# Performance work log

Hardware: AMD Instinct MI355X
Metric: run time of the kernel (lower is better)

## Reference

```python
import jax, jax.numpy as jnp
import numpy as np

HEAD_DIM = 64
N_Q_HEADS = 32
N_KV_HEADS = 8
EXPAND = N_Q_HEADS // N_KV_HEADS  # 4
ROPE_THETA = 10000.0
COMP_RATIO = 0.5
VOCAB = 32000
D_MODEL = 2048


def rotate_half(x):
    x1, x2 = jnp.split(x, 2, axis=-1)
    return jnp.concatenate([-x2, x1], axis=-1)


def setup_inputs() -> dict:
    key = jax.random.key(0)
    k0, k1, k2, k3 = jax.random.split(key, 4)
    input_ids = jax.random.randint(k0, (1, 2048), 0, VOCAB, dtype=jnp.int64)
    embed_table = jax.random.normal(k1, (VOCAB, D_MODEL), dtype=jnp.float32) * 0.02
    Wq = jax.random.normal(k2, (N_Q_HEADS * HEAD_DIM, D_MODEL), dtype=jnp.float32) * 0.02
    Wk = jax.random.normal(k3, (N_KV_HEADS * HEAD_DIM, D_MODEL), dtype=jnp.float32) * 0.02
    return {"input_ids": input_ids, "embed_table": embed_table, "Wq": Wq, "Wk": Wk}


def reference(input_ids, embed_table, Wq, Wk):
    B, S = input_ids.shape
    x = embed_table[input_ids]  # [B,S,D]

    # projections (torch Linear: x @ W.T), split heads -> [B,H,S,hd]
    q = jnp.einsum('bsd,ed->bse', x, Wq).reshape(B, S, N_Q_HEADS, HEAD_DIM).transpose(0, 2, 1, 3)
    k = jnp.einsum('bsd,ed->bse', x, Wk).reshape(B, S, N_KV_HEADS, HEAD_DIM).transpose(0, 2, 1, 3)

    # Llama RoPE, position_ids = arange(S)
    pos = jnp.arange(S, dtype=jnp.float32)
    inv_freq = 1.0 / (ROPE_THETA ** (jnp.arange(0, HEAD_DIM, 2, dtype=jnp.float32) / HEAD_DIM))
    freqs = pos[:, None] * inv_freq[None, :]                 # [S, hd/2]
    emb = jnp.concatenate([freqs, freqs], axis=-1)           # [S, hd]
    cos = jnp.cos(emb)[None, None]                           # [1,1,S,hd]
    sin = jnp.sin(emb)[None, None]
    q = q * cos + rotate_half(q) * sin
    k = k * cos + rotate_half(k) * sin

    # GQA expansion (repeat_interleave over head dim)
    k = jnp.repeat(k, EXPAND, axis=1)                        # [B,Hq,S,hd]

    # NOTE: original applies NO 1/sqrt(head_dim) scaling and NO causal mask to scores
    scores = jnp.einsum('bhqd,bhkd->bhqk', q, k)             # [B,H,S,S]
    attn = jax.nn.softmax(scores, axis=-1)

    importance = attn.mean(axis=1).mean(axis=1)[0]           # [S]

    klen = max(int(S * COMP_RATIO), 2)
    _, topk_ids = jax.lax.top_k(importance, klen)
    topk_ids = jnp.sort(topk_ids)
    # static-shape version of the "append last token if missing" branch:
    # always append S-1 (duplicate if already selected)
    topk_full = jnp.concatenate([topk_ids, jnp.array([S - 1], dtype=topk_ids.dtype)])
    pruned = jnp.take_along_axis(input_ids, topk_full[None, :], axis=1)
    return pruned, topk_full
```

## Files before the change

### kernel.cpp

```cpp
#include <hip/hip_runtime.h>
#include <math.h>

#define S       2048
#define D       2048
#define EQ      2048
#define EK      512
#define ETOT    2560
#define NH      32
#define NKV     8
#define HD      64
#define KLEN    1024

#define OFF_COS   ((size_t)0)
#define OFF_SIN   ((size_t)(256u << 10))
#define OFF_QK    ((size_t)(1u << 20))
#define OFF_KF1   ((size_t)(22u << 20))
#define OFF_KF2   ((size_t)(24u << 20))
#define OFF_PART  ((size_t)(26u << 20))
#define OFF_VALS  ((size_t)(34u << 20))
#define OFF_FLAGS ((size_t)((34u << 20) + (16u << 10)))
#define OFF_ACCP  ((size_t)((34u << 20) + (32u << 10)))

__global__ void trig_kernel(float* __restrict__ cosT, float* __restrict__ sinT) {
  int idx = blockIdx.x * blockDim.x + threadIdx.x;
  int s = idx >> 5, i = idx & 31;
  double invf = 1.0 / pow(10000.0, (double)i / 32.0);
  double ang = (double)s * invf;
  cosT[idx] = (float)cos(ang);
  sinT[idx] = (float)sin(ang);
}

#define PBM 128
#define PBN 128
#define PBK 32
#define NKT (D / PBK)

typedef _Float16 f16x8 __attribute__((ext_vector_type(8)));
typedef float    f32x4 __attribute__((ext_vector_type(4)));

__global__ __launch_bounds__(256, 2) void proj_gemm_mfma(
    const int* __restrict__ ids, const float* __restrict__ embed,
    const float* __restrict__ Wq, const float* __restrict__ Wk,
    float* __restrict__ C) {
  __shared__ __attribute__((aligned(16))) _Float16 sA[2][2][PBM * PBK];
  __shared__ __attribute__((aligned(16))) _Float16 sB[2][2][PBN * PBK];
  const int t = threadIdx.x;
  const int col0 = blockIdx.x * PBN;
  const int row0 = blockIdx.y * PBM;
  const float* Wbase = (col0 < EQ) ? (Wq + (size_t)col0 * D)
                                   : (Wk + (size_t)(col0 - EQ) * D);

  const float* srcA[2];
  const float* srcB[2];
  int ldsOff[2];
#pragma unroll
  for (int q = 0; q < 2; ++q) {
    const int e = t + q * 256;
    const int lane = e & 63, rt = e >> 6;
    const int r = rt * 16 + (lane & 15);
    const int koff = (lane >> 4) * 8;
    srcA[q] = embed + (size_t)ids[row0 + r] * D + koff;
    srcB[q] = Wbase + (size_t)r * D + koff;
    ldsOff[q] = e * 8;
  }

  const int ln = t & 63, w = t >> 6;
  const int wm = w >> 1, wn = w & 1;
  const int aoff = ln * 8;

  f32x4 acc[4][4];
#pragma unroll
  for (int m = 0; m < 4; ++m)
#pragma unroll
    for (int n = 0; n < 4; ++n) {
      f32x4 z = {0.f, 0.f, 0.f, 0.f};
      acc[m][n] = z;
    }

  float4 va[2][2], vb[2][2];

  auto load_regs = [&](int k) {
#pragma unroll
    for (int q = 0; q < 2; ++q) {
      va[q][0] = *(const float4*)(srcA[q] + k);
      va[q][1] = *(const float4*)(srcA[q] + k + 4);
      vb[q][0] = *(const float4*)(srcB[q] + k);
      vb[q][1] = *(const float4*)(srcB[q] + k + 4);
    }
  };

  auto cvt_write = [&](int buf) {
#pragma unroll
    for (int q = 0; q < 2; ++q) {
      const float fa[8] = {va[q][0].x, va[q][0].y, va[q][0].z, va[q][0].w,
                           va[q][1].x, va[q][1].y, va[q][1].z, va[q][1].w};
      const float fb[8] = {vb[q][0].x, vb[q][0].y, vb[q][0].z, vb[q][0].w,
                           vb[q][1].x, vb[q][1].y, vb[q][1].z, vb[q][1].w};
      f16x8 ah1, ah2, bh1, bh2;
#pragma unroll
      for (int j = 0; j < 8; ++j) {
        float fs = fa[j] * 64.f;
        _Float16 h = (_Float16)fs;
        ah1[j] = h;
        ah2[j] = (_Float16)(fs - (float)h);
        fs = fb[j] * 64.f;
        h = (_Float16)fs;
        bh1[j] = h;
        bh2[j] = (_Float16)(fs - (float)h);
      }
      *(f16x8*)&sA[buf][0][ldsOff[q]] = ah1;
      *(f16x8*)&sA[buf][1][ldsOff[q]] = ah2;
      *(f16x8*)&sB[buf][0][ldsOff[q]] = bh1;
      *(f16x8*)&sB[buf][1][ldsOff[q]] = bh2;
    }
  };

  load_regs(0);
  cvt_write(0);
  __syncthreads();

  int cur = 0;
  for (int kt = 0; kt < NKT; ++kt) {
    const int nb = cur ^ 1;
    const bool more = (kt + 1 < NKT);
    if (more) load_regs((kt + 1) * PBK);

    f16x8 a1[4], a2[4], b1[4], b2[4];
#pragma unroll
    for (int m = 0; m < 4; ++m) {
      const int c = (wm * 4 + m) * (16 * PBK) + aoff;
      a1[m] = *(const f16x8*)&sA[cur][0][c];
      a2[m] = *(const f16x8*)&sA[cur][1][c];
    }
#pragma unroll
    for (int n = 0; n < 4; ++n) {
      const int c = (wn * 4 + n) * (16 * PBK) + aoff;
      b1[n] = *(const f16x8*)&sB[cur][0][c];
      b2[n] = *(const f16x8*)&sB[cur][1][c];
    }
#pragma unroll
    for (int m = 0; m < 4; ++m)
#pragma unroll
      for (int n = 0; n < 4; ++n) {
        acc[m][n] = __builtin_amdgcn_mfma_f32_16x16x32_f16(a1[m], b1[n], acc[m][n], 0, 0, 0);
        acc[m][n] = __builtin_amdgcn_mfma_f32_16x16x32_f16(a1[m], b2[n], acc[m][n], 0, 0, 0);
        acc[m][n] = __builtin_amdgcn_mfma_f32_16x16x32_f16(a2[m], b1[n], acc[m][n], 0, 0, 0);
      }

    if (more) cvt_write(nb);
    __syncthreads();
    cur = nb;
  }

  const float inv = 1.f / 4096.f;
  const int colb = col0 + wn * 64 + (ln & 15);
  const int rowb = row0 + wm * 64 + (ln >> 4) * 4;
#pragma unroll
  for (int m = 0; m < 4; ++m)
#pragma unroll
    for (int j = 0; j < 4; ++j) {
      float* dst = C + (size_t)(rowb + m * 16 + j) * ETOT + colb;
#pragma unroll
      for (int n = 0; n < 4; ++n) dst[n * 16] = acc[m][n][j] * inv;
    }
}

__global__ void rope_q_kernel(float* __restrict__ qk,
                              const float* __restrict__ cosT,
                              const float* __restrict__ sinT) {
  int idx = blockIdx.x * blockDim.x + threadIdx.x;
  int s = idx >> 10;
  int rem = idx & 1023;
  int h = rem >> 5, i = rem & 31;
  float c = cosT[(s << 5) + i], sn = sinT[(s << 5) + i];
  float* p = qk + (size_t)s * ETOT + h * HD + i;
  float x1 = p[0], x2 = p[32];
  p[0]  = fmaf(x1, c, -x2 * sn);
  p[32] = fmaf(x2, c,  x1 * sn);
}

__global__ __launch_bounds__(256) void rope_k_kernel(
    const float* __restrict__ qk, _Float16* __restrict__ kf1,
    _Float16* __restrict__ kf2,
    const float* __restrict__ cosT, const float* __restrict__ sinT) {
  __shared__ float tile[64][65];
  __shared__ __attribute__((aligned(16))) float rot[64][68];
  __shared__ float ct[64][33];
  __shared__ float st[64][33];
  const int kv = blockIdx.x;
  const int s0 = blockIdx.y * 64;
  const int t = threadIdx.x;
  {
    const int c = t & 63, r = t >> 6;
#pragma unroll
    for (int p = 0; p < 16; ++p)
      tile[r + 4 * p][c] = qk[(size_t)(s0 + r + 4 * p) * ETOT + EQ + kv * HD + c];
  }
  {
    const int i = t & 31, r = t >> 5;
#pragma unroll
    for (int p = 0; p < 8; ++p) {
      ct[r + 8 * p][i] = cosT[(s0 + r + 8 * p) * 32 + i];
      st[r + 8 * p][i] = sinT[(s0 + r + 8 * p) * 32 + i];
    }
  }
  __syncthreads();
  {
    const int s = t & 63, dbase = t >> 6;
#pragma unroll
    for (int p = 0; p < 16; ++p) {
      const int d = dbase + 4 * p;
      float v;
      if (d < 32) {
        const float c = ct[s][d], sn = st[s][d];
        const float x1 = tile[s][d], x2 = tile[s][d + 32];
        v = fmaf(x1, c, -x2 * sn);
      } else {
        const float c = ct[s][d - 32], sn = st[s][d - 32];
        const float x1 = tile[s][d - 32], x2 = tile[s][d];
        v = fmaf(x2, c, x1 * sn);
      }
      rot[s][d] = v;
    }
  }
  __syncthreads();
  {
    const int w = t >> 6, l = t & 63;
    const int jt_g = (s0 >> 4) + w;
    const int jl = w * 16 + (l & 15);
#pragma unroll
    for (int ks = 0; ks < 2; ++ks) {
      const int d0 = ks * 32 + (l >> 4) * 8;
      const float4 v0 = *(const float4*)&rot[jl][d0];
      const float4 v1 = *(const float4*)&rot[jl][d0 + 4];
      const float f[8] = {v0.x, v0.y, v0.z, v0.w, v1.x, v1.y, v1.z, v1.w};
      f16x8 h1, h2;
#pragma unroll
      for (int i = 0; i < 8; ++i) {
        float fs = f[i] * 64.f;
        _Float16 hh = (_Float16)fs;
        h1[i] = hh;
        h2[i] = (_Float16)(fs - (float)hh);
      }
      const size_t off = (((size_t)(kv * 128 + jt_g) * 2 + ks) * 64 + l) * 8;
      *(f16x8*)&kf1[off] = h1;
      *(f16x8*)&kf2[off] = h2;
    }
  }
}

__global__ __launch_bounds__(512) void attn_mfma2(
    const float* __restrict__ qk, const _Float16* __restrict__ kf1,
    const _Float16* __restrict__ kf2, float* __restrict__ part) {
  const int h = blockIdx.x;
  const int rb = blockIdx.y;
  const int kv = h >> 2;
  const int t = threadIdx.x;
  const int l = t & 63, w = t >> 6;
  const int lo8 = l * 8;
  __shared__ __attribute__((aligned(16))) _Float16 kbuf[4 * 2 * 2 * 64 * 8];
  __shared__ float sbuf[8][64];

  f16x8 a1[2], a2[2];
  {
    const int grow = rb * 128 + w * 16 + (l & 15);
    const float* src = qk + (size_t)grow * ETOT + h * HD + ((l >> 4) * 8);
#pragma unroll
    for (int ks = 0; ks < 2; ++ks) {
      const float4 v0 = *(const float4*)(src + ks * 32);
      const float4 v1 = *(const float4*)(src + ks * 32 + 4);
      const float f[8] = {v0.x, v0.y, v0.z, v0.w, v1.x, v1.y, v1.z, v1.w};
#pragma unroll
      for (int i = 0; i < 8; ++i) {
        float fs = f[i] * 64.f;
        _Float16 hh = (_Float16)fs;
        a1[ks][i] = hh;
        a2[ks][i] = (_Float16)(fs - (float)hh);
      }
    }
  }

  const _Float16* gp[2];
  int ldsoff[2];
#pragma unroll
  for (int i = 0; i < 2; ++i) {
    const int c = 2 * w + i;
    const int tl = c >> 2, sp = (c >> 1) & 1, ks = c & 1;
    gp[i] = (sp ? kf2 : kf1) +
            ((size_t)((kv * 128 + tl) * 2 + ks)) * 512 + lo8;
    ldsoff[i] = ((tl * 2 + sp) * 2 + ks) * 512 + lo8;
  }

  uint4 stg0, stg1;
  auto LD = [&](int step) {
    stg0 = *(const uint4*)(gp[0] + (size_t)step * 4096);
    stg1 = *(const uint4*)(gp[1] + (size_t)step * 4096);
  };
  auto WR = [&]() {
    *(uint4*)&kbuf[ldsoff[0]] = stg0;
    *(uint4*)&kbuf[ldsoff[1]] = stg1;
  };

  float rsacc[4] = {0.f, 0.f, 0.f, 0.f};
  float invZ[4] = {0.f, 0.f, 0.f, 0.f};
  const int prow = h * 16 + rb;

  LD(0); WR();
  for (int ph = 0; ph < 2; ++ph) {
    for (int it = 0; it < 32; ++it) {
      const int nxt = (it + 1) & 31;
      const bool more = !(ph == 1 && it == 31);
      if (more) LD(nxt);
      __syncthreads();
      float v0t = 0.f, v1t = 0.f, v2t = 0.f, v3t = 0.f;
#pragma unroll
      for (int tl = 0; tl < 4; ++tl) {
        const f16x8 b1k0 = *(const f16x8*)&kbuf[((tl * 2 + 0) * 2 + 0) * 512 + lo8];
        const f16x8 b1k1 = *(const f16x8*)&kbuf[((tl * 2 + 0) * 2 + 1) * 512 + lo8];
        const f16x8 b2k0 = *(const f16x8*)&kbuf[((tl * 2 + 1) * 2 + 0) * 512 + lo8];
        const f16x8 b2k1 = *(const f16x8*)&kbuf[((tl * 2 + 1) * 2 + 1) * 512 + lo8];
        f32x4 a = {0.f, 0.f, 0.f, 0.f};
        a = __builtin_amdgcn_mfma_f32_16x16x32_f16(a1[0], b1k0, a, 0, 0, 0);
        a = __builtin_amdgcn_mfma_f32_16x16x32_f16(a1[0], b2k0, a, 0, 0, 0);
        a = __builtin_amdgcn_mfma_f32_16x16x32_f16(a2[0], b1k0, a, 0, 0, 0);
        a = __builtin_amdgcn_mfma_f32_16x16x32_f16(a1[1], b1k1, a, 0, 0, 0);
        a = __builtin_amdgcn_mfma_f32_16x16x32_f16(a1[1], b2k1, a, 0, 0, 0);
        a = __builtin_amdgcn_mfma_f32_16x16x32_f16(a2[1], b1k1, a, 0, 0, 0);
        if (ph == 0) {
#pragma unroll
          for (int r = 0; r < 4; ++r) {
            const float s = a[r] * (1.f / 4096.f);
            const float e = fmaf(s, fmaf(s, fmaf(s, fmaf(s, 1.f / 24.f, 1.f / 6.f),
                                                 0.5f), 1.f), 1.f);
            rsacc[r] += e;
          }
        } else {
          float vv = 0.f;
#pragma unroll
          for (int r = 0; r < 4; ++r) {
            const float s = a[r] * (1.f / 4096.f);
            const float e = fmaf(s, fmaf(s, fmaf(s, fmaf(s, 1.f / 24.f, 1.f / 6.f),
                                                 0.5f), 1.f), 1.f);
            vv = fmaf(e, invZ[r], vv);
          }
          if (tl == 0) v0t = vv;
          else if (tl == 1) v1t = vv;
          else if (tl == 2) v2t = vv;
          else v3t = vv;
        }
      }
      if (ph == 1) {
        float m0 = v0t + __shfl_xor(v0t, 16, 64);
        float m1 = v1t + __shfl_xor(v1t, 16, 64);
        float m2 = v2t + __shfl_xor(v2t, 16, 64);
        float m3 = v3t + __shfl_xor(v3t, 16, 64);
        const bool b4 = (l & 16) != 0;
        float a01 = b4 ? m1 : m0;
        float a23 = b4 ? m3 : m2;
        a01 += __shfl_xor(a01, 32, 64);
        a23 += __shfl_xor(a23, 32, 64);
        const float wv = (l & 32) ? a23 : a01;
        sbuf[w][l] = wv;
      }
      __syncthreads();
      if (ph == 1 && w == 0) {
        float s2 = 0.f;
#pragma unroll
        for (int ww = 0; ww < 8; ++ww) s2 += sbuf[ww][l];
        part[(size_t)prow * S + it * 64 + l] = s2;
      }
      if (more) WR();
    }
    if (ph == 0) {
#pragma unroll
      for (int r = 0; r < 4; ++r) {
#pragma unroll
        for (int off = 1; off < 16; off <<= 1)
          rsacc[r] += __shfl_xor(rsacc[r], off, 64);
        invZ[r] = 1.f / rsacc[r];
      }
    }
  }
}

__global__ void vals1_kernel(const float* __restrict__ part,
                             double* __restrict__ accp) {
  int j = blockIdx.x * 256 + threadIdx.x;
  int g = blockIdx.y;
  const float* p = part + (size_t)g * 16 * S + j;
  double s = 0.0;
  for (int b = 0; b < 16; ++b) s += (double)p[(size_t)b * S];
  accp[(size_t)g * S + j] = s;
}
__global__ void vals2_kernel(const double* __restrict__ accp,
                             double* __restrict__ vals) {
  int j = blockIdx.x * 256 + threadIdx.x;
  double s = 0.0;
  for (int g = 0; g < 32; ++g) s += accp[(size_t)g * S + j];
  vals[j] = s;
}

__global__ __launch_bounds__(256) void flags_kernel(
    const double* __restrict__ vals, int* __restrict__ flags) {
  const int j = blockIdx.x;
  const int t = threadIdx.x;
  const double v = vals[j];
  int rank = 0;
  for (int j2 = t; j2 < S; j2 += 256) {
    const double v2 = vals[j2];
    rank += (v2 > v) || (v2 == v && j2 < j);
  }
#pragma unroll
  for (int off = 32; off > 0; off >>= 1) rank += __shfl_xor(rank, off, 64);
  __shared__ int red[4];
  if ((t & 63) == 0) red[t >> 6] = rank;
  __syncthreads();
  if (t == 0)
    flags[j] = ((red[0] + red[1] + red[2] + red[3]) < KLEN) ? 1 : 0;
}

__global__ __launch_bounds__(1024) void emit_kernel(
    const int* __restrict__ flags, const int* __restrict__ ids,
    int* __restrict__ out) {
  __shared__ int fl[S];
  __shared__ int csum[32];
  __shared__ int cpre[32];
  const int t = threadIdx.x;
  for (int j = t; j < S; j += 1024) fl[j] = flags[j];
  __syncthreads();
  if (t < 32) {
    int s = 0;
    for (int i = 0; i < 64; ++i) s += fl[t * 64 + i];
    csum[t] = s;
  }
  __syncthreads();
  if (t == 0) {
    int run = 0;
    for (int c = 0; c < 32; ++c) { cpre[c] = run; run += csum[c]; }
  }
  __syncthreads();
  for (int j = t; j < S; j += 1024) {
    if (fl[j]) {
      int pos = cpre[j >> 6];
      for (int j2 = j & ~63; j2 < j; ++j2) pos += fl[j2];
      out[pos] = ids[j];
      out[KLEN + 1 + pos] = j;
    }
  }
  if (t == 0) {
    out[KLEN] = ids[S - 1];
    out[KLEN + 1 + KLEN] = S - 1;
  }
}

extern "C" void kernel_launch(void* const* d_in, const int* in_sizes, int n_in,
                              void* d_out, int out_size, void* d_ws, size_t ws_size,
                              hipStream_t stream) {
  const int* ids = (const int*)d_in[0];
  const float* embed = (const float*)d_in[1];
  const float* Wq = (const float*)d_in[2];
  const float* Wk = (const float*)d_in[3];
  int* out = (int*)d_out;
  char* ws = (char*)d_ws;
  float* cosT = (float*)(ws + OFF_COS);
  float* sinT = (float*)(ws + OFF_SIN);
  float* qk   = (float*)(ws + OFF_QK);
  _Float16* kf1 = (_Float16*)(ws + OFF_KF1);
  _Float16* kf2 = (_Float16*)(ws + OFF_KF2);
  float* part = (float*)(ws + OFF_PART);
  double* vals = (double*)(ws + OFF_VALS);
  int* flags  = (int*)(ws + OFF_FLAGS);
  double* accp = (double*)(ws + OFF_ACCP);

  trig_kernel<<<256, 256, 0, stream>>>(cosT, sinT);
  proj_gemm_mfma<<<dim3(ETOT / PBN, S / PBM), 256, 0, stream>>>(ids, embed, Wq, Wk, qk);
  rope_q_kernel<<<(S * NH * 32) / 256, 256, 0, stream>>>(qk, cosT, sinT);
  rope_k_kernel<<<dim3(NKV, S / 64), 256, 0, stream>>>(qk, kf1, kf2, cosT, sinT);
  attn_mfma2<<<dim3(NH, S / 128), 512, 0, stream>>>(qk, kf1, kf2, part);
  vals1_kernel<<<dim3(S / 256, 32), 256, 0, stream>>>(part, accp);
  vals2_kernel<<<S / 256, 256, 0, stream>>>(accp, vals);
  flags_kernel<<<S, 256, 0, stream>>>(vals, flags);
  emit_kernel<<<1, 1024, 0, stream>>>(flags, ids, out);
}
```

Measured before the change: 611.8 us.

## Shrink projection GEMM tiles to 64x64 and add XCD-aware block swizzle

Cuts the projection GEMM tile from 128x128 to 64x64, which takes the grid from 320 blocks to 1280. Raises the occupancy hint to 5 blocks per CU and remaps the 1D block index so that blocks on the same XCD share row bands, which should improve L2 reuse of embedding rows. The goal is to fill the CUs better on a grid that was too small for the machine. The cost is less reuse per tile, so global and LDS traffic rise for each MFMA issued.

After: 618.4 us. About the same (+1.1%).

```diff
diff --git a/kernel.cpp b/kernel.cpp
--- a/kernel.cpp
+++ b/kernel.cpp
@@ -30,89 +30,85 @@
   sinT[idx] = (float)sin(ang);
 }
 
-#define PBM 128
-#define PBN 128
+#define PBM 64
+#define PBN 64
 #define PBK 32
 #define NKT (D / PBK)
 
 typedef _Float16 f16x8 __attribute__((ext_vector_type(8)));
 typedef float    f32x4 __attribute__((ext_vector_type(4)));
 
-__global__ __launch_bounds__(256, 2) void proj_gemm_mfma(
+__global__ __launch_bounds__(256, 5) void proj_gemm_mfma(
     const int* __restrict__ ids, const float* __restrict__ embed,
     const float* __restrict__ Wq, const float* __restrict__ Wk,
     float* __restrict__ C) {
   __shared__ __attribute__((aligned(16))) _Float16 sA[2][2][PBM * PBK];
   __shared__ __attribute__((aligned(16))) _Float16 sB[2][2][PBN * PBK];
   const int t = threadIdx.x;
-  const int col0 = blockIdx.x * PBN;
-  const int row0 = blockIdx.y * PBM;
+  const int bid = blockIdx.x;
+  const int xcd = bid & 7, idx = bid >> 3;
+  const int bx = idx % 40;
+  const int by = xcd * 4 + idx / 40;
+  const int col0 = bx * PBN;
+  const int row0 = by * PBM;
   const float* Wbase = (col0 < EQ) ? (Wq + (size_t)col0 * D)
                                    : (Wk + (size_t)(col0 - EQ) * D);
 
-  const float* srcA[2];
-  const float* srcB[2];
-  int ldsOff[2];
-#pragma unroll
-  for (int q = 0; q < 2; ++q) {
-    const int e = t + q * 256;
-    const int lane = e & 63, rt = e >> 6;
+  const float* srcA;
+  const float* srcB;
+  int ldsOff;
+  {
+    const int lane = t & 63, rt = t >> 6;
     const int r = rt * 16 + (lane & 15);
     const int koff = (lane >> 4) * 8;
-    srcA[q] = embed + (size_t)ids[row0 + r] * D + koff;
-    srcB[q] = Wbase + (size_t)r * D + koff;
-    ldsOff[q] = e * 8;
+    srcA = embed + (size_t)ids[row0 + r] * D + koff;
+    srcB = Wbase + (size_t)r * D + koff;
+    ldsOff = t * 8;
   }
 
   const int ln = t & 63, w = t >> 6;
   const int wm = w >> 1, wn = w & 1;
   const int aoff = ln * 8;
 
-  f32x4 acc[4][4];
-#pragma unroll
-  for (int m = 0; m < 4; ++m)
-#pragma unroll
-    for (int n = 0; n < 4; ++n) {
+  f32x4 acc[2][2];
+#pragma unroll
+  for (int m = 0; m < 2; ++m)
+#pragma unroll
+    for (int n = 0; n < 2; ++n) {
       f32x4 z = {0.f, 0.f, 0.f, 0.f};
       acc[m][n] = z;
     }
 
-  float4 va[2][2], vb[2][2];
+  float4 va[2], vb[2];
 
   auto load_regs = [&](int k) {
-#pragma unroll
-    for (int q = 0; q < 2; ++q) {
-      va[q][0] = *(const float4*)(srcA[q] + k);
-      va[q][1] = *(const float4*)(srcA[q] + k + 4);
-      vb[q][0] = *(const float4*)(srcB[q] + k);
-      vb[q][1] = *(const float4*)(srcB[q] + k + 4);
-    }
+    va[0] = *(const float4*)(srcA + k);
+    va[1] = *(const float4*)(srcA + k + 4);
+    vb[0] = *(const float4*)(srcB + k);
+    vb[1] = *(const float4*)(srcB + k + 4);
   };
 
   auto cvt_write = [&](int buf) {
-#pragma unroll
-    for (int q = 0; q < 2; ++q) {
-      const float fa[8] = {va[q][0].x, va[q][0].y, va[q][0].z, va[q][0].w,
-                           va[q][1].x, va[q][1].y, va[q][1].z, va[q][1].w};
-      const float fb[8] = {vb[q][0].x, vb[q][0].y, vb[q][0].z, vb[q][0].w,
-                           vb[q][1].x, vb[q][1].y, vb[q][1].z, vb[q][1].w};
-      f16x8 ah1, ah2, bh1, bh2;
-#pragma unroll
-      for (int j = 0; j < 8; ++j) {
-        float fs = fa[j] * 64.f;
-        _Float16 h = (_Float16)fs;
-        ah1[j] = h;
-        ah2[j] = (_Float16)(fs - (float)h);
-        fs = fb[j] * 64.f;
-        h = (_Float16)fs;
-        bh1[j] = h;
-        bh2[j] = (_Float16)(fs - (float)h);
-      }
-      *(f16x8*)&sA[buf][0][ldsOff[q]] = ah1;
-      *(f16x8*)&sA[buf][1][ldsOff[q]] = ah2;
-      *(f16x8*)&sB[buf][0][ldsOff[q]] = bh1;
-      *(f16x8*)&sB[buf][1][ldsOff[q]] = bh2;
-    }
+    const float fa[8] = {va[0].x, va[0].y, va[0].z, va[0].w,
+                         va[1].x, va[1].y, va[1].z, va[1].w};
+    const float fb[8] = {vb[0].x, vb[0].y, vb[0].z, vb[0].w,
+                         vb[1].x, vb[1].y, vb[1].z, vb[1].w};
+    f16x8 ah1, ah2, bh1, bh2;
+#pragma unroll
+    for (int j = 0; j < 8; ++j) {
+      float fs = fa[j] * 64.f;
+      _Float16 h = (_Float16)fs;
+      ah1[j] = h;
+      ah2[j] = (_Float16)(fs - (float)h);
+      fs = fb[j] * 64.f;
+      h = (_Float16)fs;
+      bh1[j] = h;
+      bh2[j] = (_Float16)(fs - (float)h);
+    }
+    *(f16x8*)&sA[buf][0][ldsOff] = ah1;
+    *(f16x8*)&sA[buf][1][ldsOff] = ah2;
+    *(f16x8*)&sB[buf][0][ldsOff] = bh1;
+    *(f16x8*)&sB[buf][1][ldsOff] = bh2;
   };
 
   load_regs(0);
@@ -125,23 +121,23 @@
     const bool more = (kt + 1 < NKT);
     if (more) load_regs((kt + 1) * PBK);
 
-    f16x8 a1[4], a2[4], b1[4], b2[4];
-#pragma unroll
-    for (int m = 0; m < 4; ++m) {
-      const int c = (wm * 4 + m) * (16 * PBK) + aoff;
+    f16x8 a1[2], a2[2], b1[2], b2[2];
+#pragma unroll
+    for (int m = 0; m < 2; ++m) {
+      const int c = (wm * 2 + m) * (16 * PBK) + aoff;
       a1[m] = *(const f16x8*)&sA[cur][0][c];
       a2[m] = *(const f16x8*)&sA[cur][1][c];
     }
 #pragma unroll
-    for (int n = 0; n < 4; ++n) {
-      const int c = (wn * 4 + n) * (16 * PBK) + aoff;
+    for (int n = 0; n < 2; ++n) {
+      const int c = (wn * 2 + n) * (16 * PBK) + aoff;
       b1[n] = *(const f16x8*)&sB[cur][0][c];
       b2[n] = *(const f16x8*)&sB[cur][1][c];
     }
 #pragma unroll
-    for (int m = 0; m < 4; ++m)
-#pragma unroll
-      for (int n = 0; n < 4; ++n) {
+    for (int m = 0; m < 2; ++m)
+#pragma unroll
+      for (int n = 0; n < 2; ++n) {
         acc[m][n] = __builtin_amdgcn_mfma_f32_16x16x32_f16(a1[m], b1[n], acc[m][n], 0, 0, 0);
         acc[m][n] = __builtin_amdgcn_mfma_f32_16x16x32_f16(a1[m], b2[n], acc[m][n], 0, 0, 0);
         acc[m][n] = __builtin_amdgcn_mfma_f32_16x16x32_f16(a2[m], b1[n], acc[m][n], 0, 0, 0);
@@ -153,15 +149,15 @@
   }
 
   const float inv = 1.f / 4096.f;
-  const int colb = col0 + wn * 64 + (ln & 15);
-  const int rowb = row0 + wm * 64 + (ln >> 4) * 4;
-#pragma unroll
-  for (int m = 0; m < 4; ++m)
+  const int colb = col0 + wn * 32 + (ln & 15);
+  const int rowb = row0 + wm * 32 + (ln >> 4) * 4;
+#pragma unroll
+  for (int m = 0; m < 2; ++m)
 #pragma unroll
     for (int j = 0; j < 4; ++j) {
       float* dst = C + (size_t)(rowb + m * 16 + j) * ETOT + colb;
 #pragma unroll
-      for (int n = 0; n < 4; ++n) dst[n * 16] = acc[m][n][j] * inv;
+      for (int n = 0; n < 2; ++n) dst[n * 16] = acc[m][n][j] * inv;
     }
 }
 
@@ -473,7 +469,7 @@
   double* accp = (double*)(ws + OFF_ACCP);
 
   trig_kernel<<<256, 256, 0, stream>>>(cosT, sinT);
-  proj_gemm_mfma<<<dim3(ETOT / PBN, S / PBM), 256, 0, stream>>>(ids, embed, Wq, Wk, qk);
+  proj_gemm_mfma<<<(S / PBM) * (ETOT / PBN), 256, 0, stream>>>(ids, embed, Wq, Wk, qk);
   rope_q_kernel<<<(S * NH * 32) / 256, 256, 0, stream>>>(qk, cosT, sinT);
   rope_k_kernel<<<dim3(NKV, S / 64), 256, 0, stream>>>(qk, kf1, kf2, cosT, sinT);
   attn_mfma2<<<dim3(NH, S / 128), 512, 0, stream>>>(qk, kf1, kf2, part);
```
